# Kernel tuning notes

Measured on AMD Instinct MI355X. Metric: run time of the kernel, lower is better.

## Reference

```python
import jax, jax.numpy as jnp
import numpy as np


def conv1x1(x, W, b):
    # x: [B, C, H, W], W: [O, C], b: [O] -> [B, O, H, W]
    return jnp.einsum('bchw,oc->bohw', x, W) + b[None, :, None, None]


def setup_inputs() -> dict:
    key = jax.random.key(0)
    ks = jax.random.split(key, 8)
    B, C, H, W = 8, 128, 64, 64
    d = C // 8
    s = 0.05
    return {
        'x': jax.random.normal(ks[0], (B, C, H, W), jnp.float32),
        'Wq': jax.random.normal(ks[1], (d, C), jnp.float32) * s,
        'bq': jax.random.normal(ks[2], (d,), jnp.float32) * s,
        'Wk': jax.random.normal(ks[3], (d, C), jnp.float32) * s,
        'bk': jax.random.normal(ks[4], (d,), jnp.float32) * s,
        'Wv': jax.random.normal(ks[5], (C, C), jnp.float32) * s,
        'bv': jax.random.normal(ks[6], (C,), jnp.float32) * s,
        'gamma': jax.random.normal(ks[7], (1,), jnp.float32),
    }


def reference(x, Wq, bq, Wk, bk, Wv, bv, gamma):
    B, C, H, W = x.shape
    N = H * W
    q = conv1x1(x, Wq, bq).reshape(B, -1, N)      # [B, d, N]
    k = conv1x1(x, Wk, bk).reshape(B, -1, N)      # [B, d, N]
    v = conv1x1(x, Wv, bv).reshape(B, C, N)       # [B, C, N]
    # energy[b, i, j] = q_i . k_j  (no scaling, as in original)
    energy = jnp.einsum('bdi,bdj->bij', q, k)     # [B, N, N]
    attn = jax.nn.softmax(energy, axis=-1)
    # out[b, c, i] = sum_j v[b, c, j] * attn[b, i, j]
    out = jnp.einsum('bcj,bij->bci', v, attn).reshape(B, C, H, W)
    return gamma[0] * out + x
```

## Files before the change

kernel.cpp:

```cpp
#include <hip/hip_runtime.h>

#define BATCH 8
#define CCH   128
#define DQK   16
#define HW    4096
#define LOG2E 1.44269504088896340736f

typedef __attribute__((ext_vector_type(8))) short bf16x8;
typedef __attribute__((ext_vector_type(4))) float f32x4;

__device__ __forceinline__ unsigned cvt_pk_bf16(float lo, float hi) {
    unsigned r;
    asm("v_cvt_pk_bf16_f32 %0, %1, %2" : "=v"(r) : "v"(lo), "v"(hi));
    return r;
}

__global__ __launch_bounds__(256) void qkv_kernel(
    const float* __restrict__ x,
    const float* __restrict__ Wq, const float* __restrict__ bq,
    const float* __restrict__ Wk, const float* __restrict__ bk,
    const float* __restrict__ Wv, const float* __restrict__ bv,
    ushort* __restrict__ qT, ushort* __restrict__ kT, ushort* __restrict__ v)
{
    const int blk = blockIdx.x;
    const int b   = blk >> 6;
    const int p0  = (blk & 63) << 6;
    const int t   = threadIdx.x;
    const int l   = t & 63;
    const int w   = t >> 6;
    const int lm  = l & 15;
    const int lg  = l >> 4;

    __shared__ __align__(16) ushort W_l[160 * 136];
    __shared__ __align__(16) ushort xT_l[64 * 136];
    __shared__ float bias_l[160];

    for (int it = 0; it < 40; it++) {
        const int o  = w + 4 * it;
        const int c2 = l * 2;
        const float* src;
        float scale = 1.f;
        if (o < 16)      { src = Wq + o * CCH;        scale = LOG2E; }
        else if (o < 32) { src = Wk + (o - 16) * CCH; }
        else             { src = Wv + (o - 32) * CCH; }
        const float2 wv = *(const float2*)(src + c2);
        *(unsigned*)&W_l[o * 136 + c2] = cvt_pk_bf16(wv.x * scale, wv.y * scale);
    }
    if (t < 160) {
        float bb;
        if (t < 16)      bb = bq[t] * LOG2E;
        else if (t < 32) bb = bk[t - 16];
        else             bb = bv[t - 32];
        bias_l[t] = bb;
    }

#pragma unroll
    for (int it = 0; it < 4; it++) {
        const int oc = w + 4 * it;
        float xr[8];
#pragma unroll
        for (int r = 0; r < 8; r++)
            xr[r] = x[((size_t)(b * CCH + oc * 8 + r)) * HW + p0 + l];
        unsigned u[4];
#pragma unroll
        for (int r = 0; r < 4; r++) u[r] = cvt_pk_bf16(xr[2 * r], xr[2 * r + 1]);
        *(bf16x8*)&xT_l[l * 136 + oc * 8] = *(bf16x8*)u;
    }
    __syncthreads();

    f32x4 acc[10];
#pragma unroll
    for (int ot = 0; ot < 10; ot++)
#pragma unroll
        for (int r = 0; r < 4; r++) acc[ot][r] = 0.f;

#pragma unroll
    for (int ks = 0; ks < 4; ks++) {
        const bf16x8 bfrag = *(const bf16x8*)&xT_l[(w * 16 + lm) * 136 + ks * 32 + lg * 8];
#pragma unroll
        for (int ot = 0; ot < 10; ot++) {
            const bf16x8 afrag = *(const bf16x8*)&W_l[(ot * 16 + lm) * 136 + ks * 32 + lg * 8];
            acc[ot] = __builtin_amdgcn_mfma_f32_16x16x32_bf16(afrag, bfrag, acc[ot], 0, 0, 0);
        }
    }

    const int px = p0 + w * 16 + lm;
#pragma unroll
    for (int ot = 0; ot < 10; ot++) {
        const int ob = ot * 16 + 4 * lg;
        const float4 bb = *(const float4*)&bias_l[ob];
        const float r0 = acc[ot][0] + bb.x, r1 = acc[ot][1] + bb.y;
        const float r2 = acc[ot][2] + bb.z, r3 = acc[ot][3] + bb.w;
        const unsigned w0 = cvt_pk_bf16(r0, r1), w1 = cvt_pk_bf16(r2, r3);
        if (ot == 0) {
            uint2 pk; pk.x = w0; pk.y = w1;
            *(uint2*)&qT[((size_t)(b * HW + px)) * DQK + ob] = pk;
        } else if (ot == 1) {
            uint2 pk; pk.x = w0; pk.y = w1;
            *(uint2*)&kT[((size_t)(b * HW + px)) * DQK + (ob - 16)] = pk;
        } else {
            const int c = ob - 32;
            v[((size_t)(b * CCH + c + 0)) * HW + px] = (ushort)(w0 & 0xffff);
            v[((size_t)(b * CCH + c + 1)) * HW + px] = (ushort)(w0 >> 16);
            v[((size_t)(b * CCH + c + 2)) * HW + px] = (ushort)(w1 & 0xffff);
            v[((size_t)(b * CCH + c + 3)) * HW + px] = (ushort)(w1 >> 16);
        }
    }
}

__global__ __launch_bounds__(256) void attn_kernel(
    const ushort* __restrict__ qT, const ushort* __restrict__ kTg,
    const ushort* __restrict__ vg, const float* __restrict__ x,
    const float* __restrict__ gamma, float* __restrict__ out)
{
    const int blk = ((blockIdx.x & 7) << 6) | (blockIdx.x >> 3);
    const int b   = blk >> 6;
    const int i0  = (blk & 63) << 6;
    const int t   = threadIdx.x;
    const int l   = t & 63;
    const int w   = t >> 6;
    const int lm  = l & 15;
    const int lg  = l >> 4;

    __shared__ __align__(16) ushort kT_l[128 * 40];
    __shared__ __align__(16) ushort v_l [128 * 128];
    __shared__ __align__(16) ushort P_l [64 * 128];

    for (int idx = t; idx < 128 * 24; idx += 256)
        kT_l[(idx / 24) * 40 + 16 + (idx % 24)] = 0;

    bf16x8 qf;
#pragma unroll
    for (int z = 0; z < 8; z++) qf[z] = 0;
    if (lg < 2)
        qf = *(const bf16x8*)(qT + ((size_t)(b * HW + i0 + 16 * w + lm)) * DQK + lg * 8);

    f32x4 zero4;
#pragma unroll
    for (int z = 0; z < 4; z++) zero4[z] = 0.f;

    f32x4 acc[8];
#pragma unroll
    for (int ct = 0; ct < 8; ct++) acc[ct] = zero4;

    float m_i = -1e30f, l_i = 0.f;

    for (int j0 = 0; j0 < HW; j0 += 128) {
        __syncthreads();

        {
            const int row = t >> 1, c8 = (t & 1) * 8;
            *(bf16x8*)&kT_l[row * 40 + c8] =
                *(const bf16x8*)(kTg + ((size_t)(b * HW + j0 + row)) * DQK + c8);
        }
#pragma unroll
        for (int it = 0; it < 8; it++) {
            const int idx = t + 256 * it;
            const int c = idx >> 4, gj = idx & 15;
            const int g = gj ^ (c & 15);
            *(bf16x8*)&v_l[c * 128 + g * 8] =
                *(const bf16x8*)(vg + ((size_t)(b * CCH + c)) * HW + j0 + gj * 8);
        }
        __syncthreads();

        f32x4 s[8];
#pragma unroll
        for (int jt = 0; jt < 8; jt++) {
            const bf16x8 kf = *(const bf16x8*)&kT_l[(jt * 16 + lm) * 40 + lg * 8];
            s[jt] = __builtin_amdgcn_mfma_f32_16x16x32_bf16(kf, qf, zero4, 0, 0, 0);
        }

        float mx = s[0][0];
#pragma unroll
        for (int jt = 0; jt < 8; jt++)
#pragma unroll
            for (int r = 0; r < 4; r++) mx = fmaxf(mx, s[jt][r]);
        mx = fmaxf(mx, __shfl_xor(mx, 16));
        mx = fmaxf(mx, __shfl_xor(mx, 32));

        float m_new, alpha;
        if (__all(mx - m_i <= 8.f)) {
            m_new = m_i; alpha = 1.f;
        } else {
            m_new = fmaxf(m_i, mx);
            alpha = exp2f(m_i - m_new);
#pragma unroll
            for (int ct = 0; ct < 8; ct++) acc[ct] *= alpha;
        }

        float sum = 0.f;
        const int prow = (16 * w + lm) * 128;
#pragma unroll
        for (int jt = 0; jt < 8; jt++) {
            const float p0f = exp2f(s[jt][0] - m_new);
            const float p1f = exp2f(s[jt][1] - m_new);
            const float p2f = exp2f(s[jt][2] - m_new);
            const float p3f = exp2f(s[jt][3] - m_new);
            sum += (p0f + p1f) + (p2f + p3f);
            uint2 pk;
            pk.x = cvt_pk_bf16(p0f, p1f);
            pk.y = cvt_pk_bf16(p2f, p3f);
            const int g = (2 * jt + (lg >> 1)) ^ lm;
            *(uint2*)&P_l[prow + g * 8 + (lg & 1) * 4] = pk;
        }
        sum += __shfl_xor(sum, 16);
        sum += __shfl_xor(sum, 32);
        l_i = l_i * alpha + sum;
        m_i = m_new;

#pragma unroll
        for (int ks = 0; ks < 4; ks++) {
            const int g = (4 * ks + lg) ^ lm;
            const bf16x8 pf = *(const bf16x8*)&P_l[prow + g * 8];
#pragma unroll
            for (int ct = 0; ct < 8; ct++) {
                const bf16x8 vf = *(const bf16x8*)&v_l[(ct * 16 + lm) * 128 + g * 8];
                acc[ct] = __builtin_amdgcn_mfma_f32_16x16x32_bf16(vf, pf, acc[ct], 0, 0, 0);
            }
        }
    }

    const float linv = 1.f / l_i;
    const float gm = gamma[0];
    const int i = 16 * w + lm;
#pragma unroll
    for (int ct = 0; ct < 8; ct++) {
#pragma unroll
        for (int r = 0; r < 4; r++) {
            const int c = ct * 16 + lg * 4 + r;
            const size_t off = ((size_t)(b * CCH + c)) * HW + i0 + i;
            out[off] = gm * (acc[ct][r] * linv) + x[off];
        }
    }
}

extern "C" void kernel_launch(void* const* d_in, const int* in_sizes, int n_in,
                              void* d_out, int out_size, void* d_ws, size_t ws_size,
                              hipStream_t stream)
{
    const float* x     = (const float*)d_in[0];
    const float* Wq    = (const float*)d_in[1];
    const float* bq    = (const float*)d_in[2];
    const float* Wk    = (const float*)d_in[3];
    const float* bk    = (const float*)d_in[4];
    const float* Wv    = (const float*)d_in[5];
    const float* bv    = (const float*)d_in[6];
    const float* gamma = (const float*)d_in[7];
    float* out = (float*)d_out;

    ushort* qT = (ushort*)d_ws;
    ushort* kT = qT + (size_t)BATCH * HW * DQK;
    ushort* v  = kT + (size_t)BATCH * HW * DQK;

    qkv_kernel<<<dim3(BATCH * (HW / 64)), dim3(256), 0, stream>>>(
        x, Wq, bq, Wk, bk, Wv, bv, qT, kT, v);
    attn_kernel<<<dim3(BATCH * (HW / 64)), dim3(256), 0, stream>>>(
        qT, kT, v, x, gamma, out);
}
```

Baseline: 187.2 us.

## Use direct global-to-LDS loads in attention, drop weight LDS staging in QKV

The attention kernel now loads K and V tiles with global_load_lds, which writes straight into LDS without passing through registers. The V swizzle is moved to the source address side, and the zero-padded K tile becomes an unpadded 16-wide tile, with the upper lanes zeroed in registers instead. The QKV kernel stops staging weights and biases in LDS and reads them from global memory straight into MFMA fragments, converting them to bf16 as it goes. It also hoists the x fragments and raises wave priority around the PV MFMA loop. The trade-offs are redundant global weight reads in every block, and possible LDS bank conflicts on the unpadded K layout.

After: 187.8 us. About the same (+0.3%).

```diff
diff --git a/kernel.cpp b/kernel.cpp
--- a/kernel.cpp
+++ b/kernel.cpp
@@ -13,6 +13,12 @@
     unsigned r;
     asm("v_cvt_pk_bf16_f32 %0, %1, %2" : "=v"(r) : "v"(lo), "v"(hi));
     return r;
+}
+
+__device__ __forceinline__ void glds16(const void* gsrc, const void* lds) {
+    auto* g = (const __attribute__((address_space(1))) unsigned int*)(unsigned long long)(uintptr_t)gsrc;
+    auto* s = (__attribute__((address_space(3))) unsigned int*)(unsigned int)(uintptr_t)lds;
+    __builtin_amdgcn_global_load_lds(g, s, 16, 0, 0);
 }
 
 __global__ __launch_bounds__(256) void qkv_kernel(
@@ -31,28 +37,7 @@
     const int lm  = l & 15;
     const int lg  = l >> 4;
 
-    __shared__ __align__(16) ushort W_l[160 * 136];
     __shared__ __align__(16) ushort xT_l[64 * 136];
-    __shared__ float bias_l[160];
-
-    for (int it = 0; it < 40; it++) {
-        const int o  = w + 4 * it;
-        const int c2 = l * 2;
-        const float* src;
-        float scale = 1.f;
-        if (o < 16)      { src = Wq + o * CCH;        scale = LOG2E; }
-        else if (o < 32) { src = Wk + (o - 16) * CCH; }
-        else             { src = Wv + (o - 32) * CCH; }
-        const float2 wv = *(const float2*)(src + c2);
-        *(unsigned*)&W_l[o * 136 + c2] = cvt_pk_bf16(wv.x * scale, wv.y * scale);
-    }
-    if (t < 160) {
-        float bb;
-        if (t < 16)      bb = bq[t] * LOG2E;
-        else if (t < 32) bb = bk[t - 16];
-        else             bb = bv[t - 32];
-        bias_l[t] = bb;
-    }
 
 #pragma unroll
     for (int it = 0; it < 4; it++) {
@@ -68,6 +53,11 @@
     }
     __syncthreads();
 
+    bf16x8 bfrag[4];
+#pragma unroll
+    for (int ks = 0; ks < 4; ks++)
+        bfrag[ks] = *(const bf16x8*)&xT_l[(w * 16 + lm) * 136 + ks * 32 + lg * 8];
+
     f32x4 acc[10];
 #pragma unroll
     for (int ot = 0; ot < 10; ot++)
@@ -75,12 +65,23 @@
         for (int r = 0; r < 4; r++) acc[ot][r] = 0.f;
 
 #pragma unroll
-    for (int ks = 0; ks < 4; ks++) {
-        const bf16x8 bfrag = *(const bf16x8*)&xT_l[(w * 16 + lm) * 136 + ks * 32 + lg * 8];
-#pragma unroll
-        for (int ot = 0; ot < 10; ot++) {
-            const bf16x8 afrag = *(const bf16x8*)&W_l[(ot * 16 + lm) * 136 + ks * 32 + lg * 8];
-            acc[ot] = __builtin_amdgcn_mfma_f32_16x16x32_bf16(afrag, bfrag, acc[ot], 0, 0, 0);
+    for (int ot = 0; ot < 10; ot++) {
+        const float* Wrow;
+        if (ot == 0)      Wrow = Wq + lm * CCH;
+        else if (ot == 1) Wrow = Wk + lm * CCH;
+        else              Wrow = Wv + (ot * 16 - 32 + lm) * CCH;
+        const float scale = (ot == 0) ? LOG2E : 1.f;
+#pragma unroll
+        for (int ks = 0; ks < 4; ks++) {
+            const float4 wa = *(const float4*)(Wrow + ks * 32 + lg * 8);
+            const float4 wb = *(const float4*)(Wrow + ks * 32 + lg * 8 + 4);
+            unsigned u[4];
+            u[0] = cvt_pk_bf16(wa.x * scale, wa.y * scale);
+            u[1] = cvt_pk_bf16(wa.z * scale, wa.w * scale);
+            u[2] = cvt_pk_bf16(wb.x * scale, wb.y * scale);
+            u[3] = cvt_pk_bf16(wb.z * scale, wb.w * scale);
+            const bf16x8 afrag = *(bf16x8*)u;
+            acc[ot] = __builtin_amdgcn_mfma_f32_16x16x32_bf16(afrag, bfrag[ks], acc[ot], 0, 0, 0);
         }
     }
 
@@ -88,7 +89,15 @@
 #pragma unroll
     for (int ot = 0; ot < 10; ot++) {
         const int ob = ot * 16 + 4 * lg;
-        const float4 bb = *(const float4*)&bias_l[ob];
+        float4 bb;
+        if (ot == 0) {
+            bb = *(const float4*)(bq + 4 * lg);
+            bb.x *= LOG2E; bb.y *= LOG2E; bb.z *= LOG2E; bb.w *= LOG2E;
+        } else if (ot == 1) {
+            bb = *(const float4*)(bk + 4 * lg);
+        } else {
+            bb = *(const float4*)(bv + (ot - 2) * 16 + 4 * lg);
+        }
         const float r0 = acc[ot][0] + bb.x, r1 = acc[ot][1] + bb.y;
         const float r2 = acc[ot][2] + bb.z, r3 = acc[ot][3] + bb.w;
         const unsigned w0 = cvt_pk_bf16(r0, r1), w1 = cvt_pk_bf16(r2, r3);
@@ -122,12 +131,22 @@
     const int lm  = l & 15;
     const int lg  = l >> 4;
 
-    __shared__ __align__(16) ushort kT_l[128 * 40];
+    __shared__ __align__(16) ushort kT_l[128 * 16];
     __shared__ __align__(16) ushort v_l [128 * 128];
     __shared__ __align__(16) ushort P_l [64 * 128];
 
-    for (int idx = t; idx < 128 * 24; idx += 256)
-        kT_l[(idx / 24) * 40 + 16 + (idx % 24)] = 0;
+    const ushort* kT_src = kTg + ((size_t)b * HW) * DQK + t * 8;
+    ushort*       kT_dst = &kT_l[t * 8];
+    const ushort* v_src[8];
+    ushort*       v_dst[8];
+#pragma unroll
+    for (int it = 0; it < 8; it++) {
+        const int idx = t + 256 * it;
+        const int c   = idx >> 4;
+        const int gs  = (idx & 15) ^ (c & 15);
+        v_src[it] = vg + ((size_t)(b * CCH + c)) * HW + gs * 8;
+        v_dst[it] = &v_l[idx * 8];
+    }
 
     bf16x8 qf;
 #pragma unroll
@@ -148,25 +167,18 @@
     for (int j0 = 0; j0 < HW; j0 += 128) {
         __syncthreads();
 
-        {
-            const int row = t >> 1, c8 = (t & 1) * 8;
-            *(bf16x8*)&kT_l[row * 40 + c8] =
-                *(const bf16x8*)(kTg + ((size_t)(b * HW + j0 + row)) * DQK + c8);
-        }
-#pragma unroll
-        for (int it = 0; it < 8; it++) {
-            const int idx = t + 256 * it;
-            const int c = idx >> 4, gj = idx & 15;
-            const int g = gj ^ (c & 15);
-            *(bf16x8*)&v_l[c * 128 + g * 8] =
-                *(const bf16x8*)(vg + ((size_t)(b * CCH + c)) * HW + j0 + gj * 8);
-        }
+        glds16(kT_src + (size_t)j0 * DQK, kT_dst);
+#pragma unroll
+        for (int it = 0; it < 8; it++)
+            glds16(v_src[it] + j0, v_dst[it]);
         __syncthreads();
 
         f32x4 s[8];
 #pragma unroll
         for (int jt = 0; jt < 8; jt++) {
-            const bf16x8 kf = *(const bf16x8*)&kT_l[(jt * 16 + lm) * 40 + lg * 8];
+            bf16x8 kf = {};
+            if (lg < 2)
+                kf = *(const bf16x8*)&kT_l[(jt * 16 + lm) * 16 + lg * 8];
             s[jt] = __builtin_amdgcn_mfma_f32_16x16x32_bf16(kf, qf, zero4, 0, 0, 0);
         }
 
@@ -208,6 +220,7 @@
         l_i = l_i * alpha + sum;
         m_i = m_new;
 
+        __builtin_amdgcn_s_setprio(1);
 #pragma unroll
         for (int ks = 0; ks < 4; ks++) {
             const int g = (4 * ks + lg) ^ lm;
@@ -218,6 +231,7 @@
                 acc[ct] = __builtin_amdgcn_mfma_f32_16x16x32_bf16(vf, pf, acc[ct], 0, 0, 0);
             }
         }
+        __builtin_amdgcn_s_setprio(0);
     }
 
     const float linv = 1.f / l_i;
```
